# Performance work log

Hardware: AMD Instinct MI355X
Metric: run time of the kernel (lower is better)

Reference implementation:

```python
import jax, jax.numpy as jnp
import numpy as np

FFT_N = 320.0  # one-sided 161-bin spectrum of a 320-point FFT


def setup_inputs() -> dict:
    key = jax.random.key(0)
    spec = jax.random.normal(key, (32, 4000, 161, 2), dtype=jnp.float32)
    return {"spec": spec}


def _frame_gain(spec):
    # spec: [B, T, F, 2] -> per-frame RMS gain g0: [B, T]
    spec_pow = jnp.sum(spec * spec, axis=-1)  # [B, T, F]
    p = (jnp.sum(spec_pow[..., 1:-1], axis=-1) * 2.0
         + spec_pow[..., 0] + spec_pow[..., -1]) / FFT_N  # [B, T]
    return jnp.sqrt(p)


def _ema_over_time(g0):
    # g[0] = g0[0]; g[n] = 0.9*g[n-1] + 0.1*g0[n]  (scan over time axis 1)
    def step(carry, x):
        c = carry * 0.9 + x * 0.1
        return c, c
    init = g0[:, 0]                       # [B]
    xs = jnp.swapaxes(g0[:, 1:], 0, 1)    # [T-1, B]
    _, outs = jax.lax.scan(step, init, xs)  # [T-1, B]
    return jnp.concatenate([g0[:, :1], jnp.swapaxes(outs, 0, 1)], axis=1)  # [B, T]


def reference(spec):
    g0 = _frame_gain(spec)                        # [B, T]
    gain = _ema_over_time(g0)[:, :, None, None]   # [B, T, 1, 1]
    new_spec = spec / (gain + 0.001)              # [B, T, F, 2]
    return new_spec, gain
```

## Files before the change

### kernel.cpp

```cpp
#include <hip/hip_runtime.h>


typedef float f32x4 __attribute__((ext_vector_type(4)));
typedef float f32x2 __attribute__((ext_vector_type(2)));

#define B_SZ 32
#define T_SZ 4000
#define FRAME_F 322
#define FRAMES (B_SZ * T_SZ)
#define N_SPEC ((size_t)FRAMES * FRAME_F)
#define EMA_W 384
#define HALO (EMA_W - 1)
#define BLOCK 256
#define CHUNK 100
#define CHUNKS_PER_B (T_SZ / CHUNK)
#define C4 (CHUNK * FRAME_F / 4)

__global__ __launch_bounds__(BLOCK) void k_frame_gain(
    const float* __restrict__ spec, float* __restrict__ g0) {
  int gtid = blockIdx.x * BLOCK + threadIdx.x;
  int wid  = gtid >> 6;
  int lane = threadIdx.x & 63;
  if (wid >= FRAMES) return;

  const float* fp = spec + (size_t)wid * FRAME_F;
  f32x4 v0 = *(const f32x4*)(fp + lane * 4);
  float s0 = v0.x * v0.x + v0.y * v0.y;
  float s1 = v0.z * v0.z + v0.w * v0.w;
  float acc = 2.0f * (s0 + s1);
  if (lane == 0) acc -= s0;
  if (lane < 16) {
    f32x4 v1 = *(const f32x4*)(fp + (64 + lane) * 4);
    acc += 2.0f * (v1.x * v1.x + v1.y * v1.y + v1.z * v1.z + v1.w * v1.w);
  } else if (lane == 16) {
    f32x2 v2 = *(const f32x2*)(fp + 320);
    acc += v2.x * v2.x + v2.y * v2.y;
  }
#pragma unroll
  for (int off = 32; off > 0; off >>= 1) acc += __shfl_xor(acc, off, 64);
  if (lane == 0) g0[wid] = sqrtf(acc * (1.0f / 320.0f));
}

__global__ __launch_bounds__(BLOCK) void k_ema_apply(
    const float* __restrict__ spec, const float* __restrict__ g0,
    float* __restrict__ out, float* __restrict__ gain_out) {
  __shared__ float xs[HALO + CHUNK];
  __shared__ float inv_s[CHUNK];

  int c  = blockIdx.x;
  int b  = blockIdx.y;
  int t0 = c * CHUNK;
  int lo = t0 - HALO; if (lo < 0) lo = 0;
  int n  = t0 + CHUNK - lo;
  int tid = threadIdx.x;

  const float* gb = g0 + b * T_SZ;
  for (int i = tid; i < n; i += BLOCK) xs[i] = gb[lo + i];
  __syncthreads();

  if (tid < CHUNK) {
    int t = t0 + tid;
    int s = t - HALO; if (s < 1) s = 1;
    float cc = (s == 1) ? xs[0] : 0.f;
    for (int k = s; k <= t; ++k) cc = cc * 0.9f + xs[k - lo] * 0.1f;
    gain_out[b * T_SZ + t] = cc;
    inv_s[tid] = 1.0f / (cc + 0.001f);
  }
  __syncthreads();

  size_t base4 = ((size_t)b * T_SZ + t0) * FRAME_F / 4;
  const f32x4* sp = (const f32x4*)spec + base4;
  f32x4*       op = (f32x4*)out  + base4;
#pragma unroll 4
  for (int i = tid; i < C4; i += BLOCK) {
    f32x4 v = sp[i];
    unsigned p0 = (unsigned)(2 * i);
    unsigned lf = p0 / 161u;
    unsigned r  = p0 - lf * 161u;
    unsigned lf1 = lf + (r == 160u);
    float i0 = inv_s[lf];
    float i1 = inv_s[lf1];
    f32x4 rr;
    rr.x = v.x * i0; rr.y = v.y * i0;
    rr.z = v.z * i1; rr.w = v.w * i1;
    __builtin_nontemporal_store(rr, op + i);
  }
}

extern "C" void kernel_launch(void* const* d_in, const int* in_sizes, int n_in,
                              void* d_out, int out_size, void* d_ws, size_t ws_size,
                              hipStream_t stream) {
  const float* spec = (const float*)d_in[0];
  float* out  = (float*)d_out;
  float* gain = out + N_SPEC;
  float* g0   = (float*)d_ws;

  int blocks1 = (FRAMES + 3) / 4;
  k_frame_gain<<<blocks1, BLOCK, 0, stream>>>(spec, g0);

  dim3 g23(CHUNKS_PER_B, B_SZ);
  k_ema_apply<<<g23, BLOCK, 0, stream>>>(spec, g0, out, gain);
}
```

Before: 101.2 us.

## Fuse frame-gain reduction into EMA-apply kernel with larger chunks

```diff
diff --git a/kernel.cpp b/kernel.cpp
--- a/kernel.cpp
+++ b/kernel.cpp
@@ -11,51 +11,47 @@
 #define N_SPEC ((size_t)FRAMES * FRAME_F)
 #define EMA_W 384
 #define HALO (EMA_W - 1)
-#define BLOCK 256
-#define CHUNK 100
-#define CHUNKS_PER_B (T_SZ / CHUNK)
+#define BLOCK 1024
+#define CHUNK 500
+#define NCHUNK (T_SZ / CHUNK)
 #define C4 (CHUNK * FRAME_F / 4)
+#define XS_MAX (CHUNK + HALO)
 
-__global__ __launch_bounds__(BLOCK) void k_frame_gain(
-    const float* __restrict__ spec, float* __restrict__ g0) {
-  int gtid = blockIdx.x * BLOCK + threadIdx.x;
-  int wid  = gtid >> 6;
-  int lane = threadIdx.x & 63;
-  if (wid >= FRAMES) return;
-
-  const float* fp = spec + (size_t)wid * FRAME_F;
-  f32x4 v0 = *(const f32x4*)(fp + lane * 4);
-  float s0 = v0.x * v0.x + v0.y * v0.y;
-  float s1 = v0.z * v0.z + v0.w * v0.w;
-  float acc = 2.0f * (s0 + s1);
-  if (lane == 0) acc -= s0;
-  if (lane < 16) {
-    f32x4 v1 = *(const f32x4*)(fp + (64 + lane) * 4);
-    acc += 2.0f * (v1.x * v1.x + v1.y * v1.y + v1.z * v1.z + v1.w * v1.w);
-  } else if (lane == 16) {
-    f32x2 v2 = *(const f32x2*)(fp + 320);
-    acc += v2.x * v2.x + v2.y * v2.y;
-  }
-#pragma unroll
-  for (int off = 32; off > 0; off >>= 1) acc += __shfl_xor(acc, off, 64);
-  if (lane == 0) g0[wid] = sqrtf(acc * (1.0f / 320.0f));
-}
-
-__global__ __launch_bounds__(BLOCK) void k_ema_apply(
-    const float* __restrict__ spec, const float* __restrict__ g0,
-    float* __restrict__ out, float* __restrict__ gain_out) {
-  __shared__ float xs[HALO + CHUNK];
+__global__ __launch_bounds__(BLOCK) void k_fused_all(
+    const float* __restrict__ spec, float* __restrict__ out,
+    float* __restrict__ gain_out) {
+  __shared__ float xs[XS_MAX];
   __shared__ float inv_s[CHUNK];
 
   int c  = blockIdx.x;
   int b  = blockIdx.y;
   int t0 = c * CHUNK;
   int lo = t0 - HALO; if (lo < 0) lo = 0;
-  int n  = t0 + CHUNK - lo;
-  int tid = threadIdx.x;
+  int hiF  = t0 + CHUNK;
+  int lane = threadIdx.x & 63;
+  int wv   = threadIdx.x >> 6;
+  int tid  = threadIdx.x;
 
-  const float* gb = g0 + b * T_SZ;
-  for (int i = tid; i < n; i += BLOCK) xs[i] = gb[lo + i];
+  const float* srow = spec + (size_t)b * T_SZ * FRAME_F;
+
+  for (int f = lo + wv; f < hiF; f += 16) {
+    const float* fp = srow + (size_t)f * FRAME_F;
+    f32x4 v0 = *(const f32x4*)(fp + lane * 4);
+    float s0 = v0.x * v0.x + v0.y * v0.y;
+    float s1 = v0.z * v0.z + v0.w * v0.w;
+    float acc = 2.0f * (s0 + s1);
+    if (lane == 0) acc -= s0;
+    if (lane < 16) {
+      f32x4 v1 = *(const f32x4*)(fp + (64 + lane) * 4);
+      acc += 2.0f * (v1.x * v1.x + v1.y * v1.y + v1.z * v1.z + v1.w * v1.w);
+    } else if (lane == 16) {
+      f32x2 v2 = *(const f32x2*)(fp + 320);
+      acc += v2.x * v2.x + v2.y * v2.y;
+    }
+#pragma unroll
+    for (int off = 32; off > 0; off >>= 1) acc += __shfl_xor(acc, off, 64);
+    if (lane == 0) xs[f - lo] = sqrtf(acc * (1.0f / 320.0f));
+  }
   __syncthreads();
 
   if (tid < CHUNK) {
@@ -93,11 +89,7 @@
   const float* spec = (const float*)d_in[0];
   float* out  = (float*)d_out;
   float* gain = out + N_SPEC;
-  float* g0   = (float*)d_ws;
 
-  int blocks1 = (FRAMES + 3) / 4;
-  k_frame_gain<<<blocks1, BLOCK, 0, stream>>>(spec, g0);
-
-  dim3 g23(CHUNKS_PER_B, B_SZ);
-  k_ema_apply<<<g23, BLOCK, 0, stream>>>(spec, g0, out, gain);
+  dim3 grid(NCHUNK, B_SZ);
+  k_fused_all<<<grid, BLOCK, 0, stream>>>(spec, out, gain);
 }
```

New measurement: 134.5 us. 33.0% more time.

## Process frame pairs with 8-lane groups in gain kernel, enlarge apply chunks

Applied to the files above, without the earlier changes.

```diff
diff --git a/kernel.cpp b/kernel.cpp
--- a/kernel.cpp
+++ b/kernel.cpp
@@ -12,39 +12,59 @@
 #define EMA_W 384
 #define HALO (EMA_W - 1)
 #define BLOCK 256
-#define CHUNK 100
-#define CHUNKS_PER_B (T_SZ / CHUNK)
+#define NGROUPS (FRAMES / 2)
+#define CHUNK 250
+#define NCHUNK (T_SZ / CHUNK)
 #define C4 (CHUNK * FRAME_F / 4)
+#define XS_N (HALO + CHUNK)
 
 __global__ __launch_bounds__(BLOCK) void k_frame_gain(
     const float* __restrict__ spec, float* __restrict__ g0) {
-  int gtid = blockIdx.x * BLOCK + threadIdx.x;
-  int wid  = gtid >> 6;
-  int lane = threadIdx.x & 63;
-  if (wid >= FRAMES) return;
+  int grp = (blockIdx.x * BLOCK + threadIdx.x) >> 3;
+  int sub = threadIdx.x & 7;
+  if (grp >= NGROUPS) return;
 
-  const float* fp = spec + (size_t)wid * FRAME_F;
-  f32x4 v0 = *(const f32x4*)(fp + lane * 4);
-  float s0 = v0.x * v0.x + v0.y * v0.y;
-  float s1 = v0.z * v0.z + v0.w * v0.w;
-  float acc = 2.0f * (s0 + s1);
-  if (lane == 0) acc -= s0;
-  if (lane < 16) {
-    f32x4 v1 = *(const f32x4*)(fp + (64 + lane) * 4);
-    acc += 2.0f * (v1.x * v1.x + v1.y * v1.y + v1.z * v1.z + v1.w * v1.w);
-  } else if (lane == 16) {
-    f32x2 v2 = *(const f32x2*)(fp + 320);
-    acc += v2.x * v2.x + v2.y * v2.y;
+  const float* base = spec + (size_t)grp * 644;
+  float accA = 0.f, accB = 0.f;
+  float pw0A = 0.f, pw160A = 0.f, pw0B = 0.f, pw160B = 0.f;
+
+#pragma unroll
+  for (int k = 0; k < 21; ++k) {
+    int idx = k * 8 + sub;
+    if (idx < 161) {
+      f32x4 v = *(const f32x4*)(base + idx * 4);
+      float s01 = v.x * v.x + v.y * v.y;
+      float s23 = v.z * v.z + v.w * v.w;
+      if (idx < 80) {
+        accA += s01 + s23;
+        if (idx == 0) pw0A = s01;
+      } else if (idx == 80) {
+        accA += s01; accB += s23;
+        pw160A = s01;
+        pw0B   = s23;
+      } else {
+        accB += s01 + s23;
+        if (idx == 160) pw160B = s23;
+      }
+    }
   }
 #pragma unroll
-  for (int off = 32; off > 0; off >>= 1) acc += __shfl_xor(acc, off, 64);
-  if (lane == 0) g0[wid] = sqrtf(acc * (1.0f / 320.0f));
+  for (int off = 1; off < 8; off <<= 1) {
+    accA += __shfl_xor(accA, off, 64);
+    accB += __shfl_xor(accB, off, 64);
+  }
+  if (sub == 0) {
+    f32x2 g;
+    g.x = sqrtf((2.f * accA - pw0A - pw160A) * (1.0f / 320.0f));
+    g.y = sqrtf((2.f * accB - pw0B - pw160B) * (1.0f / 320.0f));
+    *(f32x2*)(g0 + 2 * grp) = g;
+  }
 }
 
 __global__ __launch_bounds__(BLOCK) void k_ema_apply(
     const float* __restrict__ spec, const float* __restrict__ g0,
     float* __restrict__ out, float* __restrict__ gain_out) {
-  __shared__ float xs[HALO + CHUNK];
+  __shared__ float xs[XS_N];
   __shared__ float inv_s[CHUNK];
 
   int c  = blockIdx.x;
@@ -53,8 +73,8 @@
   int lo = t0 - HALO; if (lo < 0) lo = 0;
   int n  = t0 + CHUNK - lo;
   int tid = threadIdx.x;
+  const float* gb = g0 + b * T_SZ;
 
-  const float* gb = g0 + b * T_SZ;
   for (int i = tid; i < n; i += BLOCK) xs[i] = gb[lo + i];
   __syncthreads();
 
@@ -71,7 +91,7 @@
   size_t base4 = ((size_t)b * T_SZ + t0) * FRAME_F / 4;
   const f32x4* sp = (const f32x4*)spec + base4;
   f32x4*       op = (f32x4*)out  + base4;
-#pragma unroll 4
+#pragma unroll 8
   for (int i = tid; i < C4; i += BLOCK) {
     f32x4 v = sp[i];
     unsigned p0 = (unsigned)(2 * i);
@@ -95,9 +115,8 @@
   float* gain = out + N_SPEC;
   float* g0   = (float*)d_ws;
 
-  int blocks1 = (FRAMES + 3) / 4;
-  k_frame_gain<<<blocks1, BLOCK, 0, stream>>>(spec, g0);
+  k_frame_gain<<<NGROUPS * 8 / BLOCK, BLOCK, 0, stream>>>(spec, g0);
 
-  dim3 g23(CHUNKS_PER_B, B_SZ);
+  dim3 g23(NCHUNK, B_SZ);
   k_ema_apply<<<g23, BLOCK, 0, stream>>>(spec, g0, out, gain);
 }
```

Result: faster. 95.39 us (-5.7%).
